# Optimization experiments

Hardware: AMD Instinct MI355X
Metric: run time of the kernel (lower is better)

## Reference

```python
import jax, jax.numpy as jnp
import numpy as np

N_NODES = 50000
N_EDGES = 800000
D_FEAT = 128
HEADS = 8
UNITS = 32
LEAKY_ALPHA = 0.2  # tf.nn.leaky_relu default
EPS = 1e-7


def setup_inputs() -> dict:
    key = jax.random.key(0)
    k1, k2, k3, k4, k5 = jax.random.split(key, 5)
    x = jax.random.normal(k1, (N_NODES, D_FEAT), dtype=jnp.float32)
    edges = jax.random.randint(k2, (N_EDGES, 2), 0, N_NODES, dtype=jnp.int32)
    kernel = jax.random.normal(k3, (D_FEAT, HEADS * UNITS), dtype=jnp.float32) * (1.0 / np.sqrt(D_FEAT))
    ka1 = jax.random.normal(k4, (1, HEADS, UNITS), dtype=jnp.float32) * (1.0 / np.sqrt(UNITS))
    ka2 = jax.random.normal(k5, (1, HEADS, UNITS), dtype=jnp.float32) * (1.0 / np.sqrt(UNITS))
    bias = jnp.zeros((HEADS * UNITS,), dtype=jnp.float32)
    return {"x": x, "edges": edges, "kernel": kernel, "ka1": ka1, "ka2": ka2, "bias": bias}


def reference(x, edges, kernel, ka1, ka2, bias):
    # x: [N, F]; edges: [E, 2] with columns (source, target)
    n_nodes = x.shape[0]
    targets = edges[:, 1]
    sources = edges[:, 0]

    h = (x @ kernel).reshape(-1, HEADS, UNITS)  # [N, H, U]

    f_t = jnp.sum(h * ka1, axis=-1)[targets]  # [E, H]
    # Faithful to source: f_s gathers from the EDGE-level f_t by source ids
    # (original code overwrites the ka2-based node scores), so ka2 is unused.
    f_s = f_t[sources]  # [E, H]

    scores = jax.nn.leaky_relu(f_t + f_s, negative_slope=LEAKY_ALPHA)  # [E, H]
    seg_max = jax.ops.segment_max(scores, targets, num_segments=n_nodes)
    scores = jnp.exp(scores - seg_max[targets])
    denom = jax.ops.segment_sum(scores, targets, num_segments=n_nodes) + EPS
    scores = scores / denom[targets]  # segment softmax over incoming edges

    out = jax.ops.segment_sum(scores[..., None] * h[sources], targets, num_segments=n_nodes)  # [N, H, U]
    out = out.reshape(n_nodes, HEADS * UNITS)  # concat merge
    return jax.nn.elu(out + bias)
```

## Files before the change

kernel.cpp:

```cpp
#include <hip/hip_runtime.h>
#include <hip/hip_fp16.h>

#define N_NODES 50000
#define N_EDGES 800000
#define D_FEAT 128
#define HEADS 8
#define UNITS 32
#define HU (HEADS * UNITS)
#define LEAKY 0.2f
#define EPSV 1e-7f
#define NBLK 196
#define HSP 258

typedef _Float16 half8 __attribute__((ext_vector_type(8)));
typedef float f32x4 __attribute__((ext_vector_type(4)));

struct h4pk { __half2 a, b; };

#define WBLK 128
__global__ __launch_bounds__(256) void k_wt(const float* __restrict__ W,
                                            __half* __restrict__ Wt) {
    const int i = blockIdx.x * 256 + threadIdx.x;
    const int n = i >> 7, k = i & 127;
    Wt[i] = __float2half(W[k * HU + n]);
}

#define GB 1563
#define CB 12500
__global__ __launch_bounds__(64) void k_big(const float* __restrict__ x,
                                            const __half* __restrict__ Wt,
                                            const float* __restrict__ ka1,
                                            const int* __restrict__ edges,
                                            int* __restrict__ counts,
                                            int* __restrict__ rank,
                                            __half* __restrict__ h,
                                            float* __restrict__ f) {
    __shared__ __align__(16) _Float16 hs[16 * HSP];
    const int l = threadIdx.x;
    if (blockIdx.x >= GB) {
        const int e = (blockIdx.x - GB) * 64 + l;
        if (e < N_EDGES) {
            const int tgt = edges[2 * e + 1];
            rank[e] = atomicAdd(&counts[tgt], 1);
        }
        return;
    }
    const int row16 = l & 15, kg = l >> 4;
    const int rbase = blockIdx.x * 32;

    half8 a0[4], a1[4];
    const int r0 = min(rbase + row16, N_NODES - 1);
    const int r1 = min(rbase + 16 + row16, N_NODES - 1);
    const float* xp0 = x + (size_t)r0 * D_FEAT + kg * 8;
    const float* xp1 = x + (size_t)r1 * D_FEAT + kg * 8;
#pragma unroll
    for (int ks = 0; ks < 4; ++ks) {
        const float4 u0 = *reinterpret_cast<const float4*>(xp0 + ks * 32);
        const float4 v0 = *reinterpret_cast<const float4*>(xp0 + ks * 32 + 4);
        const float4 u1 = *reinterpret_cast<const float4*>(xp1 + ks * 32);
        const float4 v1 = *reinterpret_cast<const float4*>(xp1 + ks * 32 + 4);
        half8 t0, t1;
        t0[0] = (_Float16)u0.x; t0[1] = (_Float16)u0.y; t0[2] = (_Float16)u0.z; t0[3] = (_Float16)u0.w;
        t0[4] = (_Float16)v0.x; t0[5] = (_Float16)v0.y; t0[6] = (_Float16)v0.z; t0[7] = (_Float16)v0.w;
        t1[0] = (_Float16)u1.x; t1[1] = (_Float16)u1.y; t1[2] = (_Float16)u1.z; t1[3] = (_Float16)u1.w;
        t1[4] = (_Float16)v1.x; t1[5] = (_Float16)v1.y; t1[6] = (_Float16)v1.z; t1[7] = (_Float16)v1.w;
        a0[ks] = t0; a1[ks] = t1;
    }

    f32x4 acc0[16], acc1[16];
#pragma unroll
    for (int ct = 0; ct < 16; ++ct) {
        acc0[ct] = (f32x4){0.f, 0.f, 0.f, 0.f};
        acc1[ct] = (f32x4){0.f, 0.f, 0.f, 0.f};
    }

#pragma unroll
    for (int ct = 0; ct < 16; ++ct) {
        const __half* wp = Wt + (ct * 16 + row16) * D_FEAT + kg * 8;
#pragma unroll
        for (int ks = 0; ks < 4; ++ks) {
            const half8 bf = *reinterpret_cast<const half8*>(wp + ks * 32);
            acc0[ct] = __builtin_amdgcn_mfma_f32_16x16x32_f16(a0[ks], bf, acc0[ct], 0, 0, 0);
            acc1[ct] = __builtin_amdgcn_mfma_f32_16x16x32_f16(a1[ks], bf, acc1[ct], 0, 0, 0);
        }
    }

#pragma unroll
    for (int tile = 0; tile < 2; ++tile) {
        const int rb2 = rbase + tile * 16;
#pragma unroll
        for (int ct = 0; ct < 16; ++ct) {
            const int col = ct * 16 + row16;
#pragma unroll
            for (int r = 0; r < 4; ++r) {
                const f32x4 av = tile ? acc1[ct] : acc0[ct];
                hs[(kg * 4 + r) * HSP + col] = (_Float16)av[r];
            }
        }
        __syncthreads();

#pragma unroll
        for (int j = 0; j < 8; ++j) {
            const int slot = j * 64 + l;
            const int row = slot >> 5, c8 = slot & 31;
            if (rb2 + row < N_NODES) {
                const half8 v = *reinterpret_cast<const half8*>(&hs[row * HSP + c8 * 8]);
                *reinterpret_cast<half8*>(h + (size_t)(rb2 + row) * HU + c8 * 8) = v;
            }
        }

#pragma unroll
        for (int hf = 0; hf < 2; ++hf) {
            const int o = hf * 64 + l;
            const int row = o >> 3, hd = o & 7;
            if (rb2 + row < N_NODES) {
                const _Float16* hp = &hs[row * HSP + hd * UNITS];
                const float* kp = ka1 + hd * UNITS;
                float s = 0.f;
#pragma unroll
                for (int u = 0; u < UNITS; u += 8) {
                    const half8 hv = *reinterpret_cast<const half8*>(hp + u);
                    const float4 k0 = *reinterpret_cast<const float4*>(kp + u);
                    const float4 k1 = *reinterpret_cast<const float4*>(kp + u + 4);
                    s += (float)hv[0] * k0.x + (float)hv[1] * k0.y + (float)hv[2] * k0.z + (float)hv[3] * k0.w;
                    s += (float)hv[4] * k1.x + (float)hv[5] * k1.y + (float)hv[6] * k1.z + (float)hv[7] * k1.w;
                }
                f[(size_t)rb2 * HEADS + o] = s;
            }
        }
        __syncthreads();
    }
}

__global__ __launch_bounds__(256) void k_scanA(const int* __restrict__ counts,
                                               int* __restrict__ partials) {
    const int i = blockIdx.x * 256 + threadIdx.x;
    int v = (i < N_NODES) ? counts[i] : 0;
#pragma unroll
    for (int m = 32; m >= 1; m >>= 1) v += __shfl_xor(v, m);
    __shared__ int ws[4];
    if ((threadIdx.x & 63) == 0) ws[threadIdx.x >> 6] = v;
    __syncthreads();
    if (threadIdx.x == 0) partials[blockIdx.x] = ws[0] + ws[1] + ws[2] + ws[3];
}

__global__ __launch_bounds__(256) void k_scanB(int* __restrict__ partials) {
    __shared__ int s[256];
    const int t = threadIdx.x;
    const int v = (t < NBLK) ? partials[t] : 0;
    s[t] = v;
    __syncthreads();
    for (int o = 1; o < 256; o <<= 1) {
        const int u = (t >= o) ? s[t - o] : 0;
        __syncthreads();
        s[t] += u;
        __syncthreads();
    }
    if (t < NBLK) partials[t] = s[t] - v;
}

__global__ __launch_bounds__(256) void k_scanC(const int* __restrict__ counts,
                                               const int* __restrict__ partials,
                                               const int* __restrict__ edges,
                                               const float* __restrict__ f,
                                               int* __restrict__ offs,
                                               float* __restrict__ g) {
    __shared__ int s[256];
    const int t = threadIdx.x;
    const int i = blockIdx.x * 256 + t;
    const int v = (i < N_NODES) ? counts[i] : 0;
    s[t] = v;
    __syncthreads();
    for (int o = 1; o < 256; o <<= 1) {
        const int u = (t >= o) ? s[t - o] : 0;
        __syncthreads();
        s[t] += u;
        __syncthreads();
    }
    if (i < N_NODES) {
        offs[i] = partials[blockIdx.x] + s[t] - v;
        const int t2 = edges[2 * i + 1];
        const float4 A = *reinterpret_cast<const float4*>(f + (size_t)t2 * HEADS);
        const float4 B = *reinterpret_cast<const float4*>(f + (size_t)t2 * HEADS + 4);
        *reinterpret_cast<float4*>(g + (size_t)i * HEADS) = A;
        *reinterpret_cast<float4*>(g + (size_t)i * HEADS + 4) = B;
    }
}

#define EBLK 3125
__global__ __launch_bounds__(256) void k_fill(const int* __restrict__ edges,
                                              const int* __restrict__ offs,
                                              const int* __restrict__ rank,
                                              int* __restrict__ elist) {
    const int e = blockIdx.x * 256 + threadIdx.x;
    if (e >= N_EDGES) return;
    const int2 st = reinterpret_cast<const int2*>(edges)[e];
    elist[offs[st.y] + rank[e]] = st.x;
}

__global__ __launch_bounds__(256) void k_out(const __half* __restrict__ h,
                                             const int* __restrict__ elist,
                                             const float* __restrict__ f,
                                             const float* __restrict__ g,
                                             const int* __restrict__ offs,
                                             const int* __restrict__ counts,
                                             const float* __restrict__ bias,
                                             float* __restrict__ out) {
    const int n = blockIdx.x * 4 + (threadIdx.x >> 6);
    if (n >= N_NODES) return;
    const int lane = threadIdx.x & 63;
    const int head = lane >> 3;
    const int c4 = lane * 4;
    const int start = offs[n];
    const int end = start + counts[n];
    const float fn = f[(size_t)n * HEADS + head];

    float d = 0.f;
    float4 acc = make_float4(0.f, 0.f, 0.f, 0.f);

    int p = start;
    for (; p + 4 <= end; p += 4) {
        const int s0 = elist[p + 0];
        const int s1 = elist[p + 1];
        const int s2 = elist[p + 2];
        const int s3 = elist[p + 3];
        const float gz0 = g[(size_t)s0 * HEADS + head];
        const float gz1 = g[(size_t)s1 * HEADS + head];
        const float gz2 = g[(size_t)s2 * HEADS + head];
        const float gz3 = g[(size_t)s3 * HEADS + head];
        const h4pk hv0 = *reinterpret_cast<const h4pk*>(h + (size_t)s0 * HU + c4);
        const h4pk hv1 = *reinterpret_cast<const h4pk*>(h + (size_t)s1 * HU + c4);
        const h4pk hv2 = *reinterpret_cast<const h4pk*>(h + (size_t)s2 * HU + c4);
        const h4pk hv3 = *reinterpret_cast<const h4pk*>(h + (size_t)s3 * HU + c4);

        float z0 = fn + gz0; z0 = (z0 > 0.f) ? z0 : LEAKY * z0;
        float z1 = fn + gz1; z1 = (z1 > 0.f) ? z1 : LEAKY * z1;
        float z2 = fn + gz2; z2 = (z2 > 0.f) ? z2 : LEAKY * z2;
        float z3 = fn + gz3; z3 = (z3 > 0.f) ? z3 : LEAKY * z3;
        const float w0 = __expf(z0);
        const float w1 = __expf(z1);
        const float w2 = __expf(z2);
        const float w3 = __expf(z3);
        d += (w0 + w1) + (w2 + w3);

        float2 fa, fb;
        fa = __half22float2(hv0.a); fb = __half22float2(hv0.b);
        acc.x += w0 * fa.x; acc.y += w0 * fa.y; acc.z += w0 * fb.x; acc.w += w0 * fb.y;
        fa = __half22float2(hv1.a); fb = __half22float2(hv1.b);
        acc.x += w1 * fa.x; acc.y += w1 * fa.y; acc.z += w1 * fb.x; acc.w += w1 * fb.y;
        fa = __half22float2(hv2.a); fb = __half22float2(hv2.b);
        acc.x += w2 * fa.x; acc.y += w2 * fa.y; acc.z += w2 * fb.x; acc.w += w2 * fb.y;
        fa = __half22float2(hv3.a); fb = __half22float2(hv3.b);
        acc.x += w3 * fa.x; acc.y += w3 * fa.y; acc.z += w3 * fb.x; acc.w += w3 * fb.y;
    }
    for (; p < end; ++p) {
        const int s = elist[p];
        float z = fn + g[(size_t)s * HEADS + head];
        z = (z > 0.f) ? z : LEAKY * z;
        const float w = __expf(z);
        const h4pk hv = *reinterpret_cast<const h4pk*>(h + (size_t)s * HU + c4);
        const float2 fa = __half22float2(hv.a);
        const float2 fb = __half22float2(hv.b);
        d += w;
        acc.x += w * fa.x;
        acc.y += w * fa.y;
        acc.z += w * fb.x;
        acc.w += w * fb.y;
    }

    const float inv = 1.f / (d + EPSV);
    const float4 b = *reinterpret_cast<const float4*>(bias + c4);
    float v;
    float4 o;
    v = acc.x * inv + b.x; o.x = (v > 0.f) ? v : expm1f(v);
    v = acc.y * inv + b.y; o.y = (v > 0.f) ? v : expm1f(v);
    v = acc.z * inv + b.z; o.z = (v > 0.f) ? v : expm1f(v);
    v = acc.w * inv + b.w; o.w = (v > 0.f) ? v : expm1f(v);
    *reinterpret_cast<float4*>(out + (size_t)n * HU + c4) = o;
}

extern "C" void kernel_launch(void* const* d_in, const int* in_sizes, int n_in,
                              void* d_out, int out_size, void* d_ws, size_t ws_size,
                              hipStream_t stream) {
    const float* x = (const float*)d_in[0];
    const int* edges = (const int*)d_in[1];
    const float* W = (const float*)d_in[2];
    const float* ka1 = (const float*)d_in[3];
    const float* bias = (const float*)d_in[5];
    float* out = (float*)d_out;

    char* ws = (char*)d_ws;
    size_t off = 0;
    auto alloc = [&](size_t bytes) -> void* {
        void* p = ws + off;
        off = (off + bytes + 255) & ~size_t(255);
        return p;
    };
    __half* h = (__half*)alloc(sizeof(__half) * (size_t)N_NODES * HU);
    __half* Wt = (__half*)alloc(sizeof(__half) * D_FEAT * HU);
    float* f = (float*)alloc(sizeof(float) * N_NODES * HEADS);
    float* g = (float*)alloc(sizeof(float) * N_NODES * HEADS);
    int* counts = (int*)alloc(sizeof(int) * N_NODES);
    int* offs = (int*)alloc(sizeof(int) * N_NODES);
    int* partials = (int*)alloc(sizeof(int) * NBLK);
    int* rank = (int*)alloc(sizeof(int) * N_EDGES);
    int* elist = (int*)alloc(sizeof(int) * N_EDGES);

    hipMemsetAsync(counts, 0, sizeof(int) * N_NODES, stream);

    k_wt<<<WBLK, 256, 0, stream>>>(W, Wt);
    k_big<<<GB + CB, 64, 0, stream>>>(x, Wt, ka1, edges, counts, rank, h, f);
    k_scanA<<<NBLK, 256, 0, stream>>>(counts, partials);
    k_scanB<<<1, 256, 0, stream>>>(partials);
    k_scanC<<<NBLK, 256, 0, stream>>>(counts, partials, edges, f, offs, g);
    k_fill<<<EBLK, 256, 0, stream>>>(edges, offs, rank, elist);
    k_out<<<(N_NODES + 3) / 4, 256, 0, stream>>>(h, elist, f, g, offs, counts, bias, out);
}
```

Measured before the change: 150.5 us.

## Fold memset and partials scan into kernels, unroll gather by eight, split output launch

Zeroing of counts moves into the weight-transpose kernel, which drops the separate memset. The single-block partials scan is removed and each scanC block now redundantly scans all 196 partials itself. The per-node aggregation loop is unrolled to eight edges with batched index, score and feature loads so more memory requests are in flight. The output kernel is split into two launches over node halves. Fewer launches cut fixed overhead, at the cost of redundant scan work in every block and extra register pressure from the wider unroll.

Measured after the change: 151.1 us. No clear change (+0.4%).

```diff
diff --git a/kernel.cpp b/kernel.cpp
--- a/kernel.cpp
+++ b/kernel.cpp
@@ -19,10 +19,12 @@
 
 #define WBLK 128
 __global__ __launch_bounds__(256) void k_wt(const float* __restrict__ W,
-                                            __half* __restrict__ Wt) {
+                                            __half* __restrict__ Wt,
+                                            int* __restrict__ counts) {
     const int i = blockIdx.x * 256 + threadIdx.x;
     const int n = i >> 7, k = i & 127;
     Wt[i] = __float2half(W[k * HU + n]);
+    for (int j = i; j < N_NODES; j += WBLK * 256) counts[j] = 0;
 }
 
 #define GB 1563
@@ -144,29 +146,26 @@
     if (threadIdx.x == 0) partials[blockIdx.x] = ws[0] + ws[1] + ws[2] + ws[3];
 }
 
-__global__ __launch_bounds__(256) void k_scanB(int* __restrict__ partials) {
-    __shared__ int s[256];
-    const int t = threadIdx.x;
-    const int v = (t < NBLK) ? partials[t] : 0;
-    s[t] = v;
-    __syncthreads();
-    for (int o = 1; o < 256; o <<= 1) {
-        const int u = (t >= o) ? s[t - o] : 0;
-        __syncthreads();
-        s[t] += u;
-        __syncthreads();
-    }
-    if (t < NBLK) partials[t] = s[t] - v;
-}
-
 __global__ __launch_bounds__(256) void k_scanC(const int* __restrict__ counts,
                                                const int* __restrict__ partials,
                                                const int* __restrict__ edges,
                                                const float* __restrict__ f,
                                                int* __restrict__ offs,
                                                float* __restrict__ g) {
+    __shared__ int sp[256];
     __shared__ int s[256];
     const int t = threadIdx.x;
+
+    sp[t] = (t < NBLK) ? partials[t] : 0;
+    __syncthreads();
+    for (int o = 1; o < 256; o <<= 1) {
+        const int u = (t >= o) ? sp[t - o] : 0;
+        __syncthreads();
+        sp[t] += u;
+        __syncthreads();
+    }
+    const int prefix = (blockIdx.x > 0) ? sp[blockIdx.x - 1] : 0;
+
     const int i = blockIdx.x * 256 + t;
     const int v = (i < N_NODES) ? counts[i] : 0;
     s[t] = v;
@@ -178,7 +177,7 @@
         __syncthreads();
     }
     if (i < N_NODES) {
-        offs[i] = partials[blockIdx.x] + s[t] - v;
+        offs[i] = prefix + s[t] - v;
         const int t2 = edges[2 * i + 1];
         const float4 A = *reinterpret_cast<const float4*>(f + (size_t)t2 * HEADS);
         const float4 B = *reinterpret_cast<const float4*>(f + (size_t)t2 * HEADS + 4);
@@ -205,9 +204,11 @@
                                              const int* __restrict__ offs,
                                              const int* __restrict__ counts,
                                              const float* __restrict__ bias,
-                                             float* __restrict__ out) {
-    const int n = blockIdx.x * 4 + (threadIdx.x >> 6);
-    if (n >= N_NODES) return;
+                                             float* __restrict__ out,
+                                             int nbase, int ncount) {
+    const int ni = blockIdx.x * 4 + (threadIdx.x >> 6);
+    if (ni >= ncount) return;
+    const int n = nbase + ni;
     const int lane = threadIdx.x & 63;
     const int head = lane >> 3;
     const int c4 = lane * 4;
@@ -219,39 +220,47 @@
     float4 acc = make_float4(0.f, 0.f, 0.f, 0.f);
 
     int p = start;
+    for (; p + 8 <= end; p += 8) {
+        int ss[8];
+#pragma unroll
+        for (int j = 0; j < 8; ++j) ss[j] = elist[p + j];
+        float gz[8];
+#pragma unroll
+        for (int j = 0; j < 8; ++j) gz[j] = g[(size_t)ss[j] * HEADS + head];
+        h4pk hv[8];
+#pragma unroll
+        for (int j = 0; j < 8; ++j) hv[j] = *reinterpret_cast<const h4pk*>(h + (size_t)ss[j] * HU + c4);
+#pragma unroll
+        for (int j = 0; j < 8; ++j) {
+            float z = fn + gz[j];
+            z = (z > 0.f) ? z : LEAKY * z;
+            const float w = __expf(z);
+            d += w;
+            const float2 fa = __half22float2(hv[j].a);
+            const float2 fb = __half22float2(hv[j].b);
+            acc.x += w * fa.x; acc.y += w * fa.y; acc.z += w * fb.x; acc.w += w * fb.y;
+        }
+    }
     for (; p + 4 <= end; p += 4) {
-        const int s0 = elist[p + 0];
-        const int s1 = elist[p + 1];
-        const int s2 = elist[p + 2];
-        const int s3 = elist[p + 3];
-        const float gz0 = g[(size_t)s0 * HEADS + head];
-        const float gz1 = g[(size_t)s1 * HEADS + head];
-        const float gz2 = g[(size_t)s2 * HEADS + head];
-        const float gz3 = g[(size_t)s3 * HEADS + head];
-        const h4pk hv0 = *reinterpret_cast<const h4pk*>(h + (size_t)s0 * HU + c4);
-        const h4pk hv1 = *reinterpret_cast<const h4pk*>(h + (size_t)s1 * HU + c4);
-        const h4pk hv2 = *reinterpret_cast<const h4pk*>(h + (size_t)s2 * HU + c4);
-        const h4pk hv3 = *reinterpret_cast<const h4pk*>(h + (size_t)s3 * HU + c4);
-
-        float z0 = fn + gz0; z0 = (z0 > 0.f) ? z0 : LEAKY * z0;
-        float z1 = fn + gz1; z1 = (z1 > 0.f) ? z1 : LEAKY * z1;
-        float z2 = fn + gz2; z2 = (z2 > 0.f) ? z2 : LEAKY * z2;
-        float z3 = fn + gz3; z3 = (z3 > 0.f) ? z3 : LEAKY * z3;
-        const float w0 = __expf(z0);
-        const float w1 = __expf(z1);
-        const float w2 = __expf(z2);
-        const float w3 = __expf(z3);
-        d += (w0 + w1) + (w2 + w3);
-
-        float2 fa, fb;
-        fa = __half22float2(hv0.a); fb = __half22float2(hv0.b);
-        acc.x += w0 * fa.x; acc.y += w0 * fa.y; acc.z += w0 * fb.x; acc.w += w0 * fb.y;
-        fa = __half22float2(hv1.a); fb = __half22float2(hv1.b);
-        acc.x += w1 * fa.x; acc.y += w1 * fa.y; acc.z += w1 * fb.x; acc.w += w1 * fb.y;
-        fa = __half22float2(hv2.a); fb = __half22float2(hv2.b);
-        acc.x += w2 * fa.x; acc.y += w2 * fa.y; acc.z += w2 * fb.x; acc.w += w2 * fb.y;
-        fa = __half22float2(hv3.a); fb = __half22float2(hv3.b);
-        acc.x += w3 * fa.x; acc.y += w3 * fa.y; acc.z += w3 * fb.x; acc.w += w3 * fb.y;
+        int ss[4];
+#pragma unroll
+        for (int j = 0; j < 4; ++j) ss[j] = elist[p + j];
+        float gz[4];
+#pragma unroll
+        for (int j = 0; j < 4; ++j) gz[j] = g[(size_t)ss[j] * HEADS + head];
+        h4pk hv[4];
+#pragma unroll
+        for (int j = 0; j < 4; ++j) hv[j] = *reinterpret_cast<const h4pk*>(h + (size_t)ss[j] * HU + c4);
+#pragma unroll
+        for (int j = 0; j < 4; ++j) {
+            float z = fn + gz[j];
+            z = (z > 0.f) ? z : LEAKY * z;
+            const float w = __expf(z);
+            d += w;
+            const float2 fa = __half22float2(hv[j].a);
+            const float2 fb = __half22float2(hv[j].b);
+            acc.x += w * fa.x; acc.y += w * fa.y; acc.z += w * fb.x; acc.w += w * fb.y;
+        }
     }
     for (; p < end; ++p) {
         const int s = elist[p];
@@ -306,13 +315,11 @@
     int* rank = (int*)alloc(sizeof(int) * N_EDGES);
     int* elist = (int*)alloc(sizeof(int) * N_EDGES);
 
-    hipMemsetAsync(counts, 0, sizeof(int) * N_NODES, stream);
-
-    k_wt<<<WBLK, 256, 0, stream>>>(W, Wt);
+    k_wt<<<WBLK, 256, 0, stream>>>(W, Wt, counts);
     k_big<<<GB + CB, 64, 0, stream>>>(x, Wt, ka1, edges, counts, rank, h, f);
     k_scanA<<<NBLK, 256, 0, stream>>>(counts, partials);
-    k_scanB<<<1, 256, 0, stream>>>(partials);
     k_scanC<<<NBLK, 256, 0, stream>>>(counts, partials, edges, f, offs, g);
     k_fill<<<EBLK, 256, 0, stream>>>(edges, offs, rank, elist);
-    k_out<<<(N_NODES + 3) / 4, 256, 0, stream>>>(h, elist, f, g, offs, counts, bias, out);
-}
+    k_out<<<(25000 + 3) / 4, 256, 0, stream>>>(h, elist, f, g, offs, counts, bias, out, 0, 25000);
+    k_out<<<(25000 + 3) / 4, 256, 0, stream>>>(h, elist, f, g, offs, counts, bias, out, 25000, 25000);
+}
```
